# Performance work log

Hardware: AMD Instinct MI355X
Metric: run time of the kernel (lower is better)

## Reference

```python
import jax, jax.numpy as jnp
import numpy as np

K = 20
EPS = 1e-5
SLOPE = 0.2

def knn(x, k):
    # x: (B, C, N) -> (B, N, k) nearest-neighbor indices (negative sq-dist topk)
    xx = jnp.sum(x * x, axis=1)                      # (B, N)
    inner = jnp.einsum('bcn,bcm->bnm', x, x)         # (B, N, N)
    d = 2.0 * inner - xx[:, :, None] - xx[:, None, :]
    return jax.lax.top_k(d, k)[1]

def graph_feature(x, k):
    # x: (B, C, N) -> edge features (B, N, k, 2C) = [nbr - center, center]
    idx = knn(x, k)
    xt = jnp.transpose(x, (0, 2, 1))                 # (B, N, C)
    nbr = jax.vmap(lambda f, i: f[i])(xt, idx)       # (B, N, k, C)
    center = xt[:, :, None, :]
    return jnp.concatenate([nbr - center, jnp.broadcast_to(center, nbr.shape)], axis=-1)

def bn(x, g, b, axes):
    m = jnp.mean(x, axis=axes, keepdims=True)
    v = jnp.var(x, axis=axes, keepdims=True)
    shp = [1] * x.ndim; shp[1] = x.shape[1]
    return (x - m) * jax.lax.rsqrt(v + EPS) * g.reshape(shp) + b.reshape(shp)

def lrelu(x):
    return jnp.where(x >= 0, x, SLOPE * x)

def edge_conv(x, W, g, b):
    # x: (B, C, N); W: (O, 2C) -> (B, O, N)
    e = graph_feature(x, K)                          # (B, N, k, 2C)
    h = jnp.einsum('bnkc,oc->bonk', e, W)            # 1x1 conv
    h = lrelu(bn(h, g, b, axes=(0, 2, 3)))
    return jnp.max(h, axis=-1)

def setup_inputs() -> dict:
    key = jax.random.key(0)
    ks = jax.random.split(key, 8)
    B, C, NB, P = 4, 3, 16, 128
    x = jax.random.normal(ks[0], (B, C, NB, P), dtype=jnp.float32)
    def w(k, o, i):
        return jax.random.normal(k, (o, i), dtype=jnp.float32) * (1.0 / np.sqrt(i))
    d = {'x': x,
         'W1': w(ks[1], 64, 6),   'W2': w(ks[2], 64, 128),
         'W3': w(ks[3], 128, 128),'W4': w(ks[4], 256, 256),
         'W5': w(ks[5], 1024, 512)}
    for i, c in zip(range(1, 6), [64, 64, 128, 256, 1024]):
        d[f'g{i}'] = jnp.ones((c,), jnp.float32)
        d[f'b{i}'] = jnp.zeros((c,), jnp.float32)
    return d

def reference(x, W1, W2, W3, W4, W5, g1, b1, g2, b2, g3, b3, g4, b4, g5, b5):
    B, C, NB, P = x.shape
    h = x.reshape(B, C, NB * P)                      # (B, C, N)
    x1 = edge_conv(h, W1, g1, b1)                    # (B, 64, N)
    x2 = edge_conv(x1, W2, g2, b2)                   # (B, 64, N)
    x3 = edge_conv(x2, W3, g3, b3)                   # (B, 128, N)
    x4 = edge_conv(x3, W4, g4, b4)                   # (B, 256, N)
    cat = jnp.concatenate([x1, x2, x3, x4], axis=1)  # (B, 512, N)
    pf = jnp.einsum('bcn,oc->bon', cat, W5)          # (B, 1024, N)
    pf = lrelu(bn(pf, g5, b5, axes=(0, 2)))
    pf = pf.reshape(B, pf.shape[1], NB, P)           # (B, E, NB, P)
    m = jnp.max(pf, axis=-1)                         # (B, E, NB)
    group = jnp.concatenate([m, m], axis=1)          # (B, 2E, NB)
    return pf[..., 0, :], group
```

## Files before the change

kernel.cpp:

```cpp
#include <hip/hip_runtime.h>
#include <cstdint>
#include <cmath>

#define BN_ 4
#define NPTS 2048
#define KNB 20
#define TOTP (BN_ * NPTS)

typedef unsigned short u16;
typedef unsigned long long u64;
typedef short bf16x8 __attribute__((ext_vector_type(8)));
typedef u16 u16x8 __attribute__((ext_vector_type(8)));
typedef float f32x4 __attribute__((ext_vector_type(4)));

__global__ void k_transpose(const float* __restrict__ x, float* __restrict__ P0) {
  int i = blockIdx.x * 256 + threadIdx.x;
  if (i >= TOTP) return;
  int b = i / NPTS, n = i % NPTS;
#pragma unroll
  for (int c = 0; c < 3; ++c)
    P0[i * 3 + c] = x[((size_t)b * 3 + c) * NPTS + n];
}

__global__ void k_sqnorm(const float* __restrict__ base, int ld, int C, float* __restrict__ xx) {
  int i = blockIdx.x * 256 + threadIdx.x;
  if (i >= TOTP) return;
  const float* r = base + (size_t)i * ld;
  float s = 0.f;
  for (int c = 0; c < C; ++c) s = fmaf(r[c], r[c], s);
  xx[i] = s;
}

__global__ __launch_bounds__(256, 4) void k_gram64(const float* __restrict__ A_all, int lda,
                                                   int K, float* __restrict__ G4) {
  __shared__ float As[2][8][64];
  __shared__ float Bs[2][8][64];
  const int T = NPTS / 64;
  int q = blockIdx.x;
  int bi = 0;
  while (q >= T - bi) { q -= T - bi; ++bi; }
  int bj = bi + q;
  int b = blockIdx.z;
  const float* A = A_all + (size_t)b * NPTS * lda;
  float* G = G4 + (size_t)b * NPTS * NPTS;
  int tid = threadIdx.x;
  int i0 = bi * 64, m0 = bj * 64;
  int tx = tid & 15, ty = tid >> 4;
  int lr = tid >> 2;
  int lc = (tid & 3) * 2;
  const float* Arow = A + (size_t)(i0 + lr) * lda;
  const float* Brow = A + (size_t)(m0 + lr) * lda;
  float acc[4][4] = {};
  float2 pa, pb;

  pa = *(const float2*)(Arow + lc);
  pb = *(const float2*)(Brow + lc);
  As[0][lc + 0][lr] = pa.x; As[0][lc + 1][lr] = pa.y;
  Bs[0][lc + 0][lr] = pb.x; Bs[0][lc + 1][lr] = pb.y;
  __syncthreads();
  for (int k0 = 0; k0 < K; k0 += 8) {
    int cur = (k0 >> 3) & 1;
    bool more = (k0 + 8 < K);
    if (more) {
      pa = *(const float2*)(Arow + k0 + 8 + lc);
      pb = *(const float2*)(Brow + k0 + 8 + lc);
    }
#pragma unroll
    for (int k = 0; k < 8; ++k) {
      float4 a0 = *(const float4*)&As[cur][k][ty * 4];
      float4 b0 = *(const float4*)&Bs[cur][k][tx * 4];
      float ar[4] = {a0.x, a0.y, a0.z, a0.w};
      float br[4] = {b0.x, b0.y, b0.z, b0.w};
#pragma unroll
      for (int ii = 0; ii < 4; ++ii)
#pragma unroll
        for (int jj = 0; jj < 4; ++jj)
          acc[ii][jj] = fmaf(ar[ii], br[jj], acc[ii][jj]);
    }
    if (more) {
      int nxt = cur ^ 1;
      As[nxt][lc + 0][lr] = pa.x; As[nxt][lc + 1][lr] = pa.y;
      Bs[nxt][lc + 0][lr] = pb.x; Bs[nxt][lc + 1][lr] = pb.y;
    }
    __syncthreads();
  }
#pragma unroll
  for (int ii = 0; ii < 4; ++ii) {
    int row = i0 + ty * 4 + ii;
    float4 vv = {acc[ii][0], acc[ii][1], acc[ii][2], acc[ii][3]};
    *(float4*)(G + (size_t)row * NPTS + m0 + tx * 4) = vv;
  }
  if (bi != bj) {
#pragma unroll
    for (int jj = 0; jj < 4; ++jj) {
      int col = m0 + tx * 4 + jj;
      float4 vv = {acc[0][jj], acc[1][jj], acc[2][jj], acc[3][jj]};
      *(float4*)(G + (size_t)col * NPTS + i0 + ty * 4) = vv;
    }
  }
}


__device__ __forceinline__ u16 bf16_rn(float f) {
  unsigned u = __float_as_uint(f);
  unsigned r = u + 0x7fffu + ((u >> 16) & 1u);
  return (u16)(r >> 16);
}

__global__ __launch_bounds__(256) void k_split_swz(const float* __restrict__ src,
                                                   u16* __restrict__ dh,
                                                   u16* __restrict__ dl) {
  int c = blockIdx.x * 256 + threadIdx.x;
  int row = c >> 6;
  int k0 = (c & 63) << 3;
  const float4* s = (const float4*)(src + (size_t)row * 512 + k0);
  float4 v0 = s[0], v1 = s[1];
  float vv[8] = {v0.x, v0.y, v0.z, v0.w, v1.x, v1.y, v1.z, v1.w};
  u16x8 hv, lv;
#pragma unroll
  for (int e = 0; e < 8; ++e) {
    u16 h = bf16_rn(vv[e]);
    float fh = __uint_as_float((unsigned)h << 16);
    hv[e] = h;
    lv[e] = bf16_rn(vv[e] - fh);
  }
  int tr = row >> 7, rloc = row & 127, tk = k0 >> 5, ss = (k0 >> 3) & 3;
  size_t tb = ((size_t)(tr * 16 + tk)) * 4096;
  unsigned P = ((unsigned)(rloc * 64 + ss * 16)) ^ (((unsigned)(rloc & 7)) << 4);
  *(u16x8*)(dh + tb + (P >> 1)) = hv;
  *(u16x8*)(dl + tb + (P >> 1)) = lv;
}

__device__ __forceinline__ void gl2lds16(const void* g, void* l) {
  __builtin_amdgcn_global_load_lds(
      (const __attribute__((address_space(1))) unsigned int*)g,
      (__attribute__((address_space(3))) unsigned int*)l, 16, 0, 0);
}

#define MFMA16(A, B, C) __builtin_amdgcn_mfma_f32_16x16x32_bf16(A, B, C, 0, 0, 0)

__global__ __launch_bounds__(256, 2) void k_gemm_mfma(
    const u16* __restrict__ AhT, const u16* __restrict__ AlT,
    const u16* __restrict__ BhT, const u16* __restrict__ BlT,
    float* __restrict__ Cout) {
  __shared__ u16 lds[2][4][4096];
  int tid = threadIdx.x;
  int w = tid >> 6, lane = tid & 63;
  int wr = w >> 1, wc = w & 1;
  int fr = lane & 15, fs = lane >> 4;

  size_t tbA = (size_t)blockIdx.y * 16 * 4096;
  size_t tbB = (size_t)blockIdx.x * 16 * 4096;
  int lo0 = w * 512 + lane * 8;
  int lo1 = 2048 + lo0;

  auto stage = [&](int buf, int t) {
    size_t oA = tbA + (size_t)t * 4096;
    size_t oB = tbB + (size_t)t * 4096;
    gl2lds16(AhT + oA + lo0, &lds[buf][0][lo0]);
    gl2lds16(AhT + oA + lo1, &lds[buf][0][lo1]);
    gl2lds16(AlT + oA + lo0, &lds[buf][1][lo0]);
    gl2lds16(AlT + oA + lo1, &lds[buf][1][lo1]);
    gl2lds16(BhT + oB + lo0, &lds[buf][2][lo0]);
    gl2lds16(BhT + oB + lo1, &lds[buf][2][lo1]);
    gl2lds16(BlT + oB + lo0, &lds[buf][3][lo0]);
    gl2lds16(BlT + oB + lo1, &lds[buf][3][lo1]);
  };

  unsigned aoff = ((unsigned)((wr * 64 + fr) * 64 + fs * 16)) ^ (((unsigned)(fr & 7)) << 4);
  unsigned boff = ((unsigned)((wc * 64 + fr) * 64 + fs * 16)) ^ (((unsigned)(fr & 7)) << 4);

  f32x4 acc[4][4] = {};

  stage(0, 0);
  __syncthreads();
#pragma unroll 1
  for (int t = 0; t < 16; ++t) {
    int cur = t & 1;
    if (t < 15) stage(cur ^ 1, t + 1);
    bf16x8 ah[4], al[4], bh[4], bl[4];
#pragma unroll
    for (int m = 0; m < 4; ++m) {
      ah[m] = *(const bf16x8*)((const char*)&lds[cur][0][0] + aoff + m * 1024);
      al[m] = *(const bf16x8*)((const char*)&lds[cur][1][0] + aoff + m * 1024);
    }
#pragma unroll
    for (int n = 0; n < 4; ++n) {
      bh[n] = *(const bf16x8*)((const char*)&lds[cur][2][0] + boff + n * 1024);
      bl[n] = *(const bf16x8*)((const char*)&lds[cur][3][0] + boff + n * 1024);
    }
#pragma unroll
    for (int m = 0; m < 4; ++m)
#pragma unroll
      for (int n = 0; n < 4; ++n) {
        acc[m][n] = MFMA16(ah[m], bh[n], acc[m][n]);
        acc[m][n] = MFMA16(ah[m], bl[n], acc[m][n]);
        acc[m][n] = MFMA16(al[m], bh[n], acc[m][n]);
      }
    __syncthreads();
  }
  int r0 = blockIdx.y * 128 + wr * 64 + fs * 4;
  int c0 = blockIdx.x * 128 + wc * 64 + fr;
#pragma unroll
  for (int m = 0; m < 4; ++m)
#pragma unroll
    for (int n = 0; n < 4; ++n)
#pragma unroll
      for (int r = 0; r < 4; ++r)
        Cout[(size_t)(r0 + m * 16 + r) * 1024 + (c0 + n * 16)] = acc[m][n][r];
}

__global__ __launch_bounds__(256, 4) void k_gemm64(const float* __restrict__ A, int lda, int K,
                                                   const float* __restrict__ W, int mode, int O,
                                                   int twoC, float* __restrict__ Cout, int ldc) {
  __shared__ float As[2][8][64];
  __shared__ float Bs[2][8][64];
  int tid = threadIdx.x;
  int i0 = blockIdx.y * 64, j0 = blockIdx.x * 64;
  int tx = tid & 15, ty = tid >> 4;
  int lr = tid >> 2;
  int lc = (tid & 3) * 2;
  const float* ArowA = A + (size_t)(i0 + lr) * lda;
  int j = j0 + lr;
  float acc[4][4] = {};

  auto stage = [&](int buf, int k0) {
    if ((lda & 1) == 0 && k0 + lc + 2 <= K) {
      float2 av = *(const float2*)(ArowA + k0 + lc);
      As[buf][lc + 0][lr] = av.x;
      As[buf][lc + 1][lr] = av.y;
    } else {
#pragma unroll
      for (int u = 0; u < 2; ++u) {
        int k = k0 + lc + u;
        As[buf][lc + u][lr] = (k < K) ? ArowA[k] : 0.f;
      }
    }
#pragma unroll
    for (int u = 0; u < 2; ++u) {
      int k = k0 + lc + u;
      float wv = 0.f;
      if (k < K) {
        if (mode == 0) wv = W[(size_t)j * K + k];
        else if (j < O) wv = W[(size_t)j * twoC + k];
        else { const float* wr = W + (size_t)(j - O) * twoC; wv = wr[K + k] - wr[k]; }
      }
      Bs[buf][lc + u][lr] = wv;
    }
  };

  stage(0, 0);
  __syncthreads();
  for (int k0 = 0; k0 < K; k0 += 8) {
    int cur = (k0 >> 3) & 1;
    if (k0 + 8 < K) stage(cur ^ 1, k0 + 8);
#pragma unroll
    for (int k = 0; k < 8; ++k) {
      float4 a0 = *(const float4*)&As[cur][k][ty * 4];
      float4 b0 = *(const float4*)&Bs[cur][k][tx * 4];
      float ar[4] = {a0.x, a0.y, a0.z, a0.w};
      float br[4] = {b0.x, b0.y, b0.z, b0.w};
#pragma unroll
      for (int ii = 0; ii < 4; ++ii)
#pragma unroll
        for (int jj = 0; jj < 4; ++jj)
          acc[ii][jj] = fmaf(ar[ii], br[jj], acc[ii][jj]);
    }
    __syncthreads();
  }
#pragma unroll
  for (int ii = 0; ii < 4; ++ii) {
    int row = i0 + ty * 4 + ii;
    float* cr = Cout + (size_t)row * ldc + j0;
    float4 vv = {acc[ii][0], acc[ii][1], acc[ii][2], acc[ii][3]};
    *(float4*)(cr + tx * 4) = vv;
  }
}


__device__ __forceinline__ unsigned ordf(float f) {
  int u = __float_as_int(f);
  return (unsigned)(u ^ ((u >> 31) | 0x80000000));
}

__device__ __forceinline__ unsigned rowmax16(unsigned v) {
  unsigned t;
  t = (unsigned)__builtin_amdgcn_update_dpp(0, (int)v, 0xB1, 0xF, 0xF, true);
  v = v > t ? v : t;
  t = (unsigned)__builtin_amdgcn_update_dpp(0, (int)v, 0x4E, 0xF, 0xF, true);
  v = v > t ? v : t;
  t = (unsigned)__builtin_amdgcn_update_dpp(0, (int)v, 0x141, 0xF, 0xF, true);
  v = v > t ? v : t;
  t = (unsigned)__builtin_amdgcn_update_dpp(0, (int)v, 0x140, 0xF, 0xF, true);
  v = v > t ? v : t;
  return v;
}

__device__ __forceinline__ unsigned rowmin16(unsigned v) {
  unsigned t;
  t = (unsigned)__builtin_amdgcn_update_dpp(0, (int)v, 0xB1, 0xF, 0xF, true);
  v = v < t ? v : t;
  t = (unsigned)__builtin_amdgcn_update_dpp(0, (int)v, 0x4E, 0xF, 0xF, true);
  v = v < t ? v : t;
  t = (unsigned)__builtin_amdgcn_update_dpp(0, (int)v, 0x141, 0xF, 0xF, true);
  v = v < t ? v : t;
  t = (unsigned)__builtin_amdgcn_update_dpp(0, (int)v, 0x140, 0xF, 0xF, true);
  v = v < t ? v : t;
  return v;
}

__device__ __forceinline__ unsigned wave_max_u32(unsigned v) {
  v = rowmax16(v);
  unsigned r0 = (unsigned)__builtin_amdgcn_readlane((int)v, 0);
  unsigned r1 = (unsigned)__builtin_amdgcn_readlane((int)v, 16);
  unsigned r2 = (unsigned)__builtin_amdgcn_readlane((int)v, 32);
  unsigned r3 = (unsigned)__builtin_amdgcn_readlane((int)v, 48);
  unsigned a = r0 > r1 ? r0 : r1;
  unsigned b = r2 > r3 ? r2 : r3;
  return a > b ? a : b;
}

__device__ __forceinline__ unsigned wave_min_u32(unsigned v) {
  v = rowmin16(v);
  unsigned r0 = (unsigned)__builtin_amdgcn_readlane((int)v, 0);
  unsigned r1 = (unsigned)__builtin_amdgcn_readlane((int)v, 16);
  unsigned r2 = (unsigned)__builtin_amdgcn_readlane((int)v, 32);
  unsigned r3 = (unsigned)__builtin_amdgcn_readlane((int)v, 48);
  unsigned a = r0 < r1 ? r0 : r1;
  unsigned b = r2 < r3 ? r2 : r3;
  return a < b ? a : b;
}

__device__ __forceinline__ void topk_sel(const unsigned* __restrict__ vh, int lane,
                                         int* __restrict__ idxb) {
  unsigned base = ~(unsigned)lane;
  u64 k1 = 0, k2 = 0;
#pragma unroll
  for (int t = 0; t < 32; ++t) {
    u64 key = ((u64)vh[t] << 32) | (unsigned)(base - (t << 6));
    if (key > k1) { k2 = k1; k1 = key; }
    else if (key > k2) { k2 = key; }
  }
  unsigned rm = 0;
  for (int r = 0; r < KNB; ++r) {
    unsigned o1 = (unsigned)(k1 >> 32);
    unsigned g = wave_max_u32(o1);
    bool matched = (o1 == g);
    u64 bal = __ballot(matched);
    unsigned m1 = ~(unsigned)k1;
    unsigned m_win;
    if (__popcll(bal) == 1) {
      int src = (int)(__ffsll((long long)bal) - 1);
      m_win = (unsigned)__builtin_amdgcn_readlane((int)m1, src);
    } else {
      m_win = wave_min_u32(matched ? m1 : 0xFFFFFFFFu);
    }
    if (lane == 0) idxb[r] = (int)m_win;
    bool mine = matched && (m1 == m_win);
    if (mine) {
      rm |= 1u << (m_win >> 6);
      k1 = k2;
      k2 = 0;
    }
    if (__any(mine && k1 == 0)) {
      if (mine && k1 == 0) {
        u64 a = 0, c = 0;
#pragma unroll
        for (int t = 0; t < 32; ++t) {
          unsigned q = ((rm >> t) & 1u) ? 0u : vh[t];
          u64 key = ((u64)q << 32) | (unsigned)(base - (t << 6));
          if (key > a) { c = a; a = key; }
          else if (key > c) { c = key; }
        }
        k1 = a; k2 = c;
      }
    }
  }
}

__global__ __launch_bounds__(256) void k_topk(const float* __restrict__ G4,
                                              const float* __restrict__ xx,
                                              int* __restrict__ idx) {
  int tid = threadIdx.x, w = tid >> 6, lane = tid & 63;
  int b = blockIdx.y;
  int n = blockIdx.x * 4 + w;
  const float* Gr = G4 + (size_t)b * NPTS * NPTS + (size_t)n * NPTS;
  const float* xxb = xx + b * NPTS;
  int* idxb = idx + ((size_t)b * NPTS + n) * KNB;
  float xn = xxb[n];
  unsigned vh[32];
#pragma unroll
  for (int t = 0; t < 32; ++t) {
    int m = lane + (t << 6);
    vh[t] = ordf(2.f * Gr[m] - xn - xxb[m]);
  }
  topk_sel(vh, lane, idxb);
}

__global__ __launch_bounds__(256) void k_topk3(const float* __restrict__ P0,
                                               const float* __restrict__ xx,
                                               int* __restrict__ idx) {
  int tid = threadIdx.x, w = tid >> 6, lane = tid & 63;
  int b = blockIdx.y;
  int n = blockIdx.x * 4 + w;
  const float* Pb = P0 + (size_t)b * NPTS * 3;
  const float* xxb = xx + b * NPTS;
  int* idxb = idx + ((size_t)b * NPTS + n) * KNB;
  float xn0 = Pb[n * 3 + 0], xn1 = Pb[n * 3 + 1], xn2 = Pb[n * 3 + 2];
  float xn = xxb[n];
  unsigned vh[32];
#pragma unroll
  for (int t = 0; t < 32; ++t) {
    int m = lane + (t << 6);
    const float* pm = Pb + m * 3;
    float dot = fmaf(xn2, pm[2], fmaf(xn1, pm[1], fmaf(xn0, pm[0], 0.f)));
    vh[t] = ordf(2.f * dot - xn - xxb[m]);
  }
  topk_sel(vh, lane, idxb);
}

__global__ void k_gather(const float* __restrict__ YS, int twoO, int O,
                         const int* __restrict__ idx,
                         float* __restrict__ hmax, float* __restrict__ hmin,
                         double* __restrict__ Pbuf, double* __restrict__ Qbuf) {
  __shared__ float ps[4][256];
  __shared__ float pq[4][256];
  int tid = threadIdx.x, w = tid >> 6, lane = tid & 63;
  int i = blockIdx.x * 4 + w;
  int b = i / NPTS;
  int Q = O >> 6;
  float s[4], hx[4], hn[4], sm[4], sq[4];
  const float* Srow = YS + (size_t)i * twoO + O;
#pragma unroll
  for (int q = 0; q < 4; ++q) {
    if (q < Q) s[q] = Srow[lane + 64 * q];
    hx[q] = -__builtin_inff(); hn[q] = __builtin_inff(); sm[q] = 0.f; sq[q] = 0.f;
  }
  const int* ip = idx + (size_t)i * KNB;
  for (int k = 0; k < KNB; ++k) {
    int m = ip[k];
    const float* Yrow = YS + (size_t)(b * NPTS + m) * twoO;
#pragma unroll
    for (int q = 0; q < 4; ++q) {
      if (q < Q) {
        float h = Yrow[lane + 64 * q] + s[q];
        hx[q] = fmaxf(hx[q], h);
        hn[q] = fminf(hn[q], h);
        sm[q] += h;
        sq[q] = fmaf(h, h, sq[q]);
      }
    }
  }
#pragma unroll
  for (int q = 0; q < 4; ++q) {
    if (q < Q) {
      int o = lane + 64 * q;
      hmax[(size_t)i * O + o] = hx[q];
      hmin[(size_t)i * O + o] = hn[q];
      ps[w][o] = sm[q];
      pq[w][o] = sq[q];
    }
  }
  __syncthreads();
  if (tid < O) {
    double t1 = (double)(ps[0][tid] + ps[1][tid] + ps[2][tid] + ps[3][tid]);
    double t2 = (double)(pq[0][tid] + pq[1][tid] + pq[2][tid] + pq[3][tid]);
    Pbuf[(size_t)tid * 2048 + blockIdx.x] = t1;
    Qbuf[(size_t)tid * 2048 + blockIdx.x] = t2;
  }
}

__global__ __launch_bounds__(256) void k_redstats(const double* __restrict__ Pbuf,
                                                  const double* __restrict__ Qbuf,
                                                  const float* __restrict__ g,
                                                  const float* __restrict__ bb, float cnt,
                                                  float* __restrict__ scale,
                                                  float* __restrict__ shift) {
  __shared__ double s1[256], s2[256];
  int o = blockIdx.x, t = threadIdx.x;
  double a = 0.0, c = 0.0;
#pragma unroll
  for (int j = 0; j < 8; ++j) {
    a += Pbuf[(size_t)o * 2048 + t + 256 * j];
    c += Qbuf[(size_t)o * 2048 + t + 256 * j];
  }
  s1[t] = a; s2[t] = c;
  __syncthreads();
  for (int s = 128; s; s >>= 1) {
    if (t < s) { s1[t] += s1[t + s]; s2[t] += s2[t + s]; }
    __syncthreads();
  }
  if (t == 0) {
    double mean = s1[0] / (double)cnt;
    double var = s2[0] / (double)cnt - mean * mean;
    double sc = (double)g[o] / sqrt(var + 1e-5);
    scale[o] = (float)sc;
    shift[o] = (float)((double)bb[o] - mean * sc);
  }
}

__global__ void k_apply(const float* __restrict__ hmax, const float* __restrict__ hmin,
                        const float* __restrict__ scale, const float* __restrict__ shift,
                        float* __restrict__ Fout, int O) {
  int t = blockIdx.x * 256 + threadIdx.x;
  int i = t / O, o = t % O;
  float sc = scale[o];
  float h = (sc >= 0.f) ? hmax[t] : hmin[t];
  float v = fmaf(sc, h, shift[o]);
  Fout[(size_t)i * 512 + o] = (v >= 0.f) ? v : 0.2f * v;
}

__global__ void k_fstats(const float* __restrict__ PF, double* __restrict__ Fb,
                         double* __restrict__ Qb) {
  int tid = threadIdx.x, bid = blockIdx.x;
  float sm[4] = {0.f, 0.f, 0.f, 0.f}, sq[4] = {0.f, 0.f, 0.f, 0.f};
  int r0 = bid * 128;
  for (int r = 0; r < 128; ++r) {
    const float* row = PF + (size_t)(r0 + r) * 1024;
#pragma unroll
    for (int q = 0; q < 4; ++q) {
      float v = row[tid + 256 * q];
      sm[q] += v;
      sq[q] = fmaf(v, v, sq[q]);
    }
  }
#pragma unroll
  for (int q = 0; q < 4; ++q) {
    int o = tid + 256 * q;
    Fb[(size_t)o * 64 + bid] = (double)sm[q];
    Qb[(size_t)o * 64 + bid] = (double)sq[q];
  }
}

__global__ __launch_bounds__(64) void k_red5(const double* __restrict__ Fb,
                                             const double* __restrict__ Qb,
                                             const float* __restrict__ g,
                                             const float* __restrict__ bb,
                                             float* __restrict__ sc5, float* __restrict__ sh5) {
  __shared__ double s1[64], s2[64];
  int o = blockIdx.x, t = threadIdx.x;
  s1[t] = Fb[(size_t)o * 64 + t];
  s2[t] = Qb[(size_t)o * 64 + t];
  __syncthreads();
  for (int s = 32; s; s >>= 1) {
    if (t < s) { s1[t] += s1[t + s]; s2[t] += s2[t + s]; }
    __syncthreads();
  }
  if (t == 0) {
    double cnt = (double)TOTP;
    double mean = s1[0] / cnt;
    double var = s2[0] / cnt - mean * mean;
    double sc = (double)g[o] / sqrt(var + 1e-5);
    sc5[o] = (float)sc;
    sh5[o] = (float)((double)bb[o] - mean * sc);
  }
}

__global__ void k_out0(const float* __restrict__ PF, const float* __restrict__ sc5,
                       const float* __restrict__ sh5, float* __restrict__ out0) {
  __shared__ float t[64][65];
  int b = blockIdx.z, p0 = blockIdx.y * 64, o0 = blockIdx.x * 64;
  int ol = threadIdx.x & 63, pg = threadIdx.x >> 6;
#pragma unroll
  for (int q = 0; q < 16; ++q) {
    int p = q * 4 + pg;
    t[p][ol] = PF[((size_t)(b * NPTS + p0 + p)) * 1024 + o0 + ol];
  }
  __syncthreads();
#pragma unroll
  for (int q = 0; q < 16; ++q) {
    int oo = q * 4 + pg;
    int o = o0 + oo;
    float v = fmaf(sc5[o], t[ol][oo], sh5[o]);
    float a = (v >= 0.f) ? v : 0.2f * v;
    out0[((size_t)(b * 1024 + o)) * 128 + p0 + ol] = a;
  }
}

__global__ void k_gmax(const float* __restrict__ PF, const float* __restrict__ sc5,
                       const float* __restrict__ sh5, float* __restrict__ tmpmax) {
  int b = blockIdx.z, nb = blockIdx.y;
  int o = blockIdx.x * 256 + threadIdx.x;
  const float* base = PF + ((size_t)(b * NPTS + nb * 128)) * 1024 + o;
  float sc = sc5[o], sh = sh5[o];
  float m0 = -__builtin_inff(), m1 = m0, m2 = m0, m3 = m0;
  for (int p = 0; p < 128; p += 4) {
    float v0 = base[(size_t)(p + 0) * 1024];
    float v1 = base[(size_t)(p + 1) * 1024];
    float v2 = base[(size_t)(p + 2) * 1024];
    float v3 = base[(size_t)(p + 3) * 1024];
    float a0 = fmaf(sc, v0, sh); a0 = (a0 >= 0.f) ? a0 : 0.2f * a0;
    float a1 = fmaf(sc, v1, sh); a1 = (a1 >= 0.f) ? a1 : 0.2f * a1;
    float a2 = fmaf(sc, v2, sh); a2 = (a2 >= 0.f) ? a2 : 0.2f * a2;
    float a3 = fmaf(sc, v3, sh); a3 = (a3 >= 0.f) ? a3 : 0.2f * a3;
    m0 = fmaxf(m0, a0); m1 = fmaxf(m1, a1);
    m2 = fmaxf(m2, a2); m3 = fmaxf(m3, a3);
  }
  tmpmax[(size_t)(b * 16 + nb) * 1024 + o] = fmaxf(fmaxf(m0, m1), fmaxf(m2, m3));
}

__global__ void k_gdup(const float* __restrict__ tmpmax, float* __restrict__ gout) {
  __shared__ float t[16][65];
  int b = blockIdx.y, o0 = blockIdx.x * 64;
  int ol = threadIdx.x & 63, ng = threadIdx.x >> 6;
#pragma unroll
  for (int q = 0; q < 4; ++q) {
    int nb = q * 4 + ng;
    t[nb][ol] = tmpmax[(size_t)(b * 16 + nb) * 1024 + o0 + ol];
  }
  __syncthreads();
  int nb2 = threadIdx.x & 15, og = threadIdx.x >> 4;
#pragma unroll
  for (int q = 0; q < 4; ++q) {
    int oo = q * 16 + og;
    float v = t[nb2][oo];
    size_t base = ((size_t)(b * 2048) + o0 + oo) * 16 + nb2;
    gout[base] = v;
    gout[base + 1024 * 16] = v;
  }
}

extern "C" void kernel_launch(void* const* d_in, const int* in_sizes, int n_in,
                              void* d_out, int out_size, void* d_ws, size_t ws_size,
                              hipStream_t stream) {
  const float* x  = (const float*)d_in[0];
  const float* W1 = (const float*)d_in[1];
  const float* W2 = (const float*)d_in[2];
  const float* W3 = (const float*)d_in[3];
  const float* W4 = (const float*)d_in[4];
  const float* W5 = (const float*)d_in[5];
  const float* g1 = (const float*)d_in[6];  const float* b1 = (const float*)d_in[7];
  const float* g2 = (const float*)d_in[8];  const float* b2 = (const float*)d_in[9];
  const float* g3 = (const float*)d_in[10]; const float* b3 = (const float*)d_in[11];
  const float* g4 = (const float*)d_in[12]; const float* b4 = (const float*)d_in[13];
  const float* g5 = (const float*)d_in[14]; const float* b5 = (const float*)d_in[15];

  float* ws = (float*)d_ws;
  size_t off = 0;
  auto alloc = [&](size_t nfl) { float* p = ws + off; off += (nfl + 63) & ~(size_t)63; return p; };
  float*  P0   = alloc((size_t)TOTP * 3);
  float*  F    = alloc((size_t)TOTP * 512);
  float*  xx   = alloc(TOTP);
  float*  U    = alloc((size_t)BN_ * NPTS * NPTS);
  float*  G4   = U;
  float*  YS   = U;
  float*  hmax = U + (size_t)TOTP * 512;
  float*  hmin = hmax + (size_t)TOTP * 256;
  float*  PF   = hmin + (size_t)TOTP * 256;
  float*  tmpmax = alloc((size_t)BN_ * 16 * 1024);
  double* Pbuf = (double*)alloc((size_t)256 * 2048 * 2);
  double* Qbuf = (double*)alloc((size_t)256 * 2048 * 2);
  double* Fb   = (double*)alloc((size_t)1024 * 64 * 2);
  double* Qb   = (double*)alloc((size_t)1024 * 64 * 2);
  float*  scale= alloc(256);
  float*  shift= alloc(256);
  float*  sc5  = alloc(1024);
  float*  sh5  = alloc(1024);
  int*    idx  = (int*)alloc((size_t)TOTP * KNB);

  k_transpose<<<32, 256, 0, stream>>>(x, P0);

  struct L { const float* base; int lda, C, O, colout; const float* W; const float* g; const float* b; };
  L Ls[4] = {
    {P0,      3,   3,   64,  0,   W1, g1, b1},
    {F,       512, 64,  64,  64,  W2, g2, b2},
    {F + 64,  512, 64,  128, 128, W3, g3, b3},
    {F + 128, 512, 128, 256, 256, W4, g4, b4},
  };

  for (int l = 0; l < 4; ++l) {
    const L& a = Ls[l];
    k_sqnorm<<<32, 256, 0, stream>>>(a.base, a.lda, a.C, xx);
    if (l == 0) {
      k_topk3<<<dim3(512, BN_), 256, 0, stream>>>(P0, xx, idx);
    } else {
      k_gram64<<<dim3(528, 1, BN_), 256, 0, stream>>>(a.base, a.lda, a.C, G4);
      k_topk<<<dim3(512, BN_), 256, 0, stream>>>(G4, xx, idx);
    }
    int twoO = 2 * a.O;
    k_gemm64<<<dim3(twoO / 64, TOTP / 64), 256, 0, stream>>>(
        a.base, a.lda, a.C, a.W, 1, a.O, 2 * a.C, YS, twoO);
    k_gather<<<TOTP / 4, 256, 0, stream>>>(YS, twoO, a.O, idx, hmax, hmin, Pbuf, Qbuf);
    k_redstats<<<a.O, 256, 0, stream>>>(Pbuf, Qbuf, a.g, a.b, (float)(BN_ * NPTS * KNB),
                                        scale, shift);
    k_apply<<<TOTP * a.O / 256, 256, 0, stream>>>(hmax, hmin, scale, shift, F + a.colout, a.O);
  }

  u16* FhT = (u16*)U;
  u16* FlT = FhT + (size_t)4194304;
  u16* WhT = FlT + (size_t)4194304;
  u16* WlT = WhT + (size_t)524288;
  k_split_swz<<<2048, 256, 0, stream>>>(F, FhT, FlT);
  k_split_swz<<<256, 256, 0, stream>>>(W5, WhT, WlT);
  k_gemm_mfma<<<dim3(8, 64), 256, 0, stream>>>(FhT, FlT, WhT, WlT, PF);

  k_fstats<<<64, 256, 0, stream>>>(PF, Fb, Qb);
  k_red5<<<1024, 64, 0, stream>>>(Fb, Qb, g5, b5, sc5, sh5);

  float* out0 = (float*)d_out;
  float* gout = out0 + (size_t)BN_ * 1024 * 128;
  k_out0<<<dim3(16, 2, BN_), 256, 0, stream>>>(PF, sc5, sh5, out0);
  k_gmax<<<dim3(4, 16, BN_), 256, 0, stream>>>(PF, sc5, sh5, tmpmax);
  k_gdup<<<dim3(16, BN_), 256, 0, stream>>>(tmpmax, gout);
}
```

Baseline: 648.0 us.

## Coalesce gram transpose store, vectorize top-k loads, widen fstats grid

The symmetric gram kernel now writes its mirrored tile through a padded shared-memory buffer, so the transposed store becomes row-contiguous float4 writes. The top-k kernels give each lane four consecutive columns and load them with float4, which changes the index encoding in the selection routine to keep tie-breaking consistent. The feature-stats kernel is split across four column blocks to run more workgroups. The risks are extra LDS use and a sync in the gram kernel, and possible mistakes in the remapped index arithmetic.

```diff
diff --git a/kernel.cpp b/kernel.cpp
--- a/kernel.cpp
+++ b/kernel.cpp
@@ -35,6 +35,7 @@
                                                    int K, float* __restrict__ G4) {
   __shared__ float As[2][8][64];
   __shared__ float Bs[2][8][64];
+  __shared__ float tb[64][68];
   const int T = NPTS / 64;
   int q = blockIdx.x;
   int bi = 0;
@@ -93,9 +94,17 @@
   if (bi != bj) {
 #pragma unroll
     for (int jj = 0; jj < 4; ++jj) {
-      int col = m0 + tx * 4 + jj;
       float4 vv = {acc[0][jj], acc[1][jj], acc[2][jj], acc[3][jj]};
-      *(float4*)(G + (size_t)col * NPTS + i0 + ty * 4) = vv;
+      *(float4*)&tb[tx * 4 + jj][ty * 4] = vv;
+    }
+    __syncthreads();
+    int cl0 = tid >> 4;
+    int cc = (tid & 15) * 4;
+#pragma unroll
+    for (int qq = 0; qq < 4; ++qq) {
+      int cl = qq * 16 + cl0;
+      float4 vv = *(const float4*)&tb[cl][cc];
+      *(float4*)(G + (size_t)(m0 + cl) * NPTS + i0 + cc) = vv;
     }
   }
 }
@@ -331,13 +340,13 @@
   return a < b ? a : b;
 }
 
-__device__ __forceinline__ void topk_sel(const unsigned* __restrict__ vh, int lane,
-                                         int* __restrict__ idxb) {
-  unsigned base = ~(unsigned)lane;
+__device__ __forceinline__ void topk_sel_c(const unsigned* __restrict__ vh, int lane,
+                                           int* __restrict__ idxb) {
+  unsigned base = ~(unsigned)(lane * 4);
   u64 k1 = 0, k2 = 0;
 #pragma unroll
   for (int t = 0; t < 32; ++t) {
-    u64 key = ((u64)vh[t] << 32) | (unsigned)(base - (t << 6));
+    u64 key = ((u64)vh[t] << 32) | (unsigned)(base - ((t >> 2) * 256 + (t & 3)));
     if (key > k1) { k2 = k1; k1 = key; }
     else if (key > k2) { k2 = key; }
   }
@@ -358,7 +367,7 @@
     if (lane == 0) idxb[r] = (int)m_win;
     bool mine = matched && (m1 == m_win);
     if (mine) {
-      rm |= 1u << (m_win >> 6);
+      rm |= 1u << (((m_win >> 8) << 2) | (m_win & 3));
       k1 = k2;
       k2 = 0;
     }
@@ -368,7 +377,7 @@
 #pragma unroll
         for (int t = 0; t < 32; ++t) {
           unsigned q = ((rm >> t) & 1u) ? 0u : vh[t];
-          u64 key = ((u64)q << 32) | (unsigned)(base - (t << 6));
+          u64 key = ((u64)q << 32) | (unsigned)(base - ((t >> 2) * 256 + (t & 3)));
           if (key > a) { c = a; a = key; }
           else if (key > c) { c = key; }
         }
@@ -388,13 +397,19 @@
   const float* xxb = xx + b * NPTS;
   int* idxb = idx + ((size_t)b * NPTS + n) * KNB;
   float xn = xxb[n];
+  int mb = lane * 4;
   unsigned vh[32];
 #pragma unroll
-  for (int t = 0; t < 32; ++t) {
-    int m = lane + (t << 6);
-    vh[t] = ordf(2.f * Gr[m] - xn - xxb[m]);
-  }
-  topk_sel(vh, lane, idxb);
+  for (int t4 = 0; t4 < 8; ++t4) {
+    int m0 = t4 * 256 + mb;
+    float4 gv = *(const float4*)(Gr + m0);
+    float4 xv = *(const float4*)(xxb + m0);
+    vh[t4 * 4 + 0] = ordf(2.f * gv.x - xn - xv.x);
+    vh[t4 * 4 + 1] = ordf(2.f * gv.y - xn - xv.y);
+    vh[t4 * 4 + 2] = ordf(2.f * gv.z - xn - xv.z);
+    vh[t4 * 4 + 3] = ordf(2.f * gv.w - xn - xv.w);
+  }
+  topk_sel_c(vh, lane, idxb);
 }
 
 __global__ __launch_bounds__(256) void k_topk3(const float* __restrict__ P0,
@@ -408,15 +423,26 @@
   int* idxb = idx + ((size_t)b * NPTS + n) * KNB;
   float xn0 = Pb[n * 3 + 0], xn1 = Pb[n * 3 + 1], xn2 = Pb[n * 3 + 2];
   float xn = xxb[n];
+  int mb = lane * 4;
   unsigned vh[32];
 #pragma unroll
-  for (int t = 0; t < 32; ++t) {
-    int m = lane + (t << 6);
-    const float* pm = Pb + m * 3;
-    float dot = fmaf(xn2, pm[2], fmaf(xn1, pm[1], fmaf(xn0, pm[0], 0.f)));
-    vh[t] = ordf(2.f * dot - xn - xxb[m]);
-  }
-  topk_sel(vh, lane, idxb);
+  for (int t4 = 0; t4 < 8; ++t4) {
+    int m0 = t4 * 256 + mb;
+    const float* pm = Pb + (size_t)m0 * 3;
+    float4 f0 = *(const float4*)(pm + 0);
+    float4 f1 = *(const float4*)(pm + 4);
+    float4 f2 = *(const float4*)(pm + 8);
+    float4 xv = *(const float4*)(xxb + m0);
+    float d0 = fmaf(xn2, f0.z, fmaf(xn1, f0.y, fmaf(xn0, f0.x, 0.f)));
+    float d1 = fmaf(xn2, f1.y, fmaf(xn1, f1.x, fmaf(xn0, f0.w, 0.f)));
+    float d2 = fmaf(xn2, f2.x, fmaf(xn1, f1.w, fmaf(xn0, f1.z, 0.f)));
+    float d3 = fmaf(xn2, f2.w, fmaf(xn1, f2.z, fmaf(xn0, f2.y, 0.f)));
+    vh[t4 * 4 + 0] = ordf(2.f * d0 - xn - xv.x);
+    vh[t4 * 4 + 1] = ordf(2.f * d1 - xn - xv.y);
+    vh[t4 * 4 + 2] = ordf(2.f * d2 - xn - xv.z);
+    vh[t4 * 4 + 3] = ordf(2.f * d3 - xn - xv.w);
+  }
+  topk_sel_c(vh, lane, idxb);
 }
 
 __global__ void k_gather(const float* __restrict__ YS, int twoO, int O,
@@ -513,23 +539,16 @@
 __global__ void k_fstats(const float* __restrict__ PF, double* __restrict__ Fb,
                          double* __restrict__ Qb) {
   int tid = threadIdx.x, bid = blockIdx.x;
-  float sm[4] = {0.f, 0.f, 0.f, 0.f}, sq[4] = {0.f, 0.f, 0.f, 0.f};
+  int o = blockIdx.y * 256 + tid;
+  float sm = 0.f, sq = 0.f;
   int r0 = bid * 128;
   for (int r = 0; r < 128; ++r) {
-    const float* row = PF + (size_t)(r0 + r) * 1024;
-#pragma unroll
-    for (int q = 0; q < 4; ++q) {
-      float v = row[tid + 256 * q];
-      sm[q] += v;
-      sq[q] = fmaf(v, v, sq[q]);
-    }
-  }
-#pragma unroll
-  for (int q = 0; q < 4; ++q) {
-    int o = tid + 256 * q;
-    Fb[(size_t)o * 64 + bid] = (double)sm[q];
-    Qb[(size_t)o * 64 + bid] = (double)sq[q];
-  }
+    float v = PF[(size_t)(r0 + r) * 1024 + o];
+    sm += v;
+    sq = fmaf(v, v, sq);
+  }
+  Fb[(size_t)o * 64 + bid] = (double)sm;
+  Qb[(size_t)o * 64 + bid] = (double)sq;
 }
 
 __global__ __launch_bounds__(64) void k_red5(const double* __restrict__ Fb,
@@ -694,7 +713,7 @@
   k_split_swz<<<256, 256, 0, stream>>>(W5, WhT, WlT);
   k_gemm_mfma<<<dim3(8, 64), 256, 0, stream>>>(FhT, FlT, WhT, WlT, PF);
 
-  k_fstats<<<64, 256, 0, stream>>>(PF, Fb, Qb);
+  k_fstats<<<dim3(64, 4), 256, 0, stream>>>(PF, Fb, Qb);
   k_red5<<<1024, 64, 0, stream>>>(Fb, Qb, g5, b5, sc5, sh5);
 
   float* out0 = (float*)d_out;
```

After: 620.4 us. 1.04x faster.
